# Performance work log

Hardware: AMD Instinct MI355X
Metric: run time of the kernel (lower is better)

## Reference

```python
import jax, jax.numpy as jnp
import numpy as np

SEQ_LEN = 12
BATCH = 2048
IN_DIM = 512
HIDDEN = 1024


def setup_inputs() -> dict:
    key = jax.random.key(0)
    k1, k2, k3, k4 = jax.random.split(key, 4)
    scale = 1.0 / np.sqrt(IN_DIM + HIDDEN)
    return {
        "x": jax.random.normal(k1, (BATCH, SEQ_LEN, IN_DIM), dtype=jnp.float32),
        "coded_cords": jax.random.normal(k2, (BATCH, HIDDEN), dtype=jnp.float32),
        # TF GRUCell fused gate kernel: [in+hidden, 2*hidden] (reset, update), bias init 1.0
        "gate_kernel": jax.random.normal(k3, (IN_DIM + HIDDEN, 2 * HIDDEN), dtype=jnp.float32) * scale,
        "gate_bias": jnp.ones((2 * HIDDEN,), dtype=jnp.float32),
        # candidate kernel: [in+hidden, hidden], zero bias
        "cand_kernel": jax.random.normal(k4, (IN_DIM + HIDDEN, HIDDEN), dtype=jnp.float32) * scale,
        "cand_bias": jnp.zeros((HIDDEN,), dtype=jnp.float32),
    }


def reference(x, coded_cords, gate_kernel, gate_bias, cand_kernel, cand_bias):
    # GRU recurrence (tf.contrib.rnn.GRUCell math), initial state = coded_cords.
    def step(h, xt):
        # xt: [B, D], h: [B, H]
        gates = jax.nn.sigmoid(jnp.concatenate([xt, h], axis=-1) @ gate_kernel + gate_bias)
        r, u = jnp.split(gates, 2, axis=-1)  # reset, update gates [B, H]
        c = jnp.tanh(jnp.concatenate([xt, r * h], axis=-1) @ cand_kernel + cand_bias)
        h_new = u * h + (1.0 - u) * c
        return h_new, h_new

    xs = jnp.swapaxes(x, 0, 1)  # [T, B, D]
    _, ys = jax.lax.scan(step, coded_cords, xs)  # ys: [T, B, H]
    return jnp.swapaxes(ys, 0, 1)  # [B, T, H]
```

## Files before the change

### kernel.cpp

```cpp
#include <hip/hip_runtime.h>
#include <hip/hip_bf16.h>


#define T_SEQ 12
#define BATCH 2048
#define IND 512
#define HID 1024
#define NGATE (2 * HID)
#define NPRE (NGATE + HID)

typedef __bf16 bf16x8 __attribute__((ext_vector_type(8)));
typedef __bf16 bf16x4 __attribute__((ext_vector_type(4)));
typedef float floatx4 __attribute__((ext_vector_type(4)));

#define AS1 __attribute__((address_space(1)))
#define AS3 __attribute__((address_space(3)))

__device__ __forceinline__ void gload16(const __bf16* g, __bf16* l) {
  __builtin_amdgcn_global_load_lds((const AS1 void*)g, (AS3 void*)l, 16, 0, 0);
}

__device__ __forceinline__ float fast_sigmoid(float v) {
  v = fminf(30.f, fmaxf(-30.f, v));
  return 1.f / (1.f + __expf(-v));
}
__device__ __forceinline__ float fast_tanh(float v) {
  v = fminf(15.f, fmaxf(-15.f, v));
  float e = __expf(2.f * v);
  return (e - 1.f) / (e + 1.f);
}

__global__ __launch_bounds__(256) void prep(
    const float* __restrict__ Wg, const float* __restrict__ Wc,
    const float* __restrict__ x, const float* __restrict__ coded,
    __bf16* __restrict__ Bx, __bf16* __restrict__ Bhg, __bf16* __restrict__ Bhc,
    __bf16* __restrict__ xb, float* __restrict__ h32, __bf16* __restrict__ hb) {
  int b = blockIdx.x;
  if (b < 2304) {
    int gid = b * 256 + threadIdx.x;
    int g = gid >> 6, lane = gid & 63;
    const float* W; int ld, row0, ksteps, wid; __bf16* out;
    if (g < 2048)      { W = Wg; ld = NGATE; row0 = 0;   ksteps = 16; wid = g;        out = Bx; }
    else if (g < 3072) { W = Wc; ld = HID;   row0 = 0;   ksteps = 16; wid = g - 2048; out = Bx + (size_t)2048 * 512; }
    else if (g < 7168) { W = Wg; ld = NGATE; row0 = IND; ksteps = 32; wid = g - 3072; out = Bhg; }
    else               { W = Wc; ld = HID;   row0 = IND; ksteps = 32; wid = g - 7168; out = Bhc; }
    int n16 = wid / ksteps, kt = wid - n16 * ksteps;
    int col = n16 * 16 + (lane & 15);
    int k0 = row0 + kt * 32 + (lane >> 4) * 8;
    bf16x8 v;
#pragma unroll
    for (int j = 0; j < 8; ++j) v[j] = (__bf16)W[(size_t)(k0 + j) * ld + col];
    *reinterpret_cast<bf16x8*>(out + (size_t)wid * 512 + lane * 8) = v;
  } else if (b < 4352) {
    int i = (b - 2304) * 256 + threadIdx.x;
    const float4* x4 = (const float4*)x;
    const int n4 = BATCH * T_SEQ * IND / 4;
    for (int k = i; k < n4; k += 2048 * 256) {
      float4 v = x4[k];
      bf16x4 o;
      o[0] = (__bf16)v.x; o[1] = (__bf16)v.y; o[2] = (__bf16)v.z; o[3] = (__bf16)v.w;
      *reinterpret_cast<bf16x4*>(xb + (size_t)k * 4) = o;
    }
  } else {
    int i = (b - 4352) * 256 + threadIdx.x;
    float4 v = ((const float4*)coded)[i];
    ((float4*)h32)[i] = v;
    bf16x4 o;
    o[0] = (__bf16)v.x; o[1] = (__bf16)v.y; o[2] = (__bf16)v.z; o[3] = (__bf16)v.w;
    *reinterpret_cast<bf16x4*>(hb + (size_t)i * 4) = o;
  }
}

__global__ __launch_bounds__(256) void pre_gemm(
    const __bf16* __restrict__ xb, const __bf16* __restrict__ Bx,
    const float* __restrict__ bg, const float* __restrict__ bc,
    __bf16* __restrict__ Pg, __bf16* __restrict__ Pc) {
  __shared__ __bf16 Alds[128 * 64];
  __shared__ __bf16 Blds[8192];
  const int tid = threadIdx.x, lane = tid & 63, w = tid >> 6;
  const int wm = w >> 1, wn = w & 1, quad = lane >> 4, l16 = lane & 15;
  const int bid = blockIdx.x;
  const int wg = (bid & 7) * 576 + (bid >> 3);
  const int nb = wg % 24;
  const int rest = wg / 24;
  const int mB = rest & 15;
  const int tz = rest >> 4;
  const int m0 = mB * 128;

  const __bf16* gA[4]; __bf16* lA[4];
  const __bf16* gB[4]; __bf16* lB[4];
#pragma unroll
  for (int i = 0; i < 4; ++i) {
    int c = tid + i * 256;
    int row = c >> 3, k8 = c & 7;
    gA[i] = xb + ((size_t)(m0 + row) * T_SEQ + tz) * IND + ((k8 ^ (row & 7)) * 8);
    lA[i] = Alds + c * 8;
    int ks2c = c >> 9, rem = c & 511;
    gB[i] = Bx + (((size_t)(nb * 8 + (rem >> 6)) * 16 + ks2c) * 64 + (rem & 63)) * 8;
    lB[i] = Blds + c * 8;
  }

  floatx4 acc[4][4] = {};
  for (int it = 0; it < 8; ++it) {
    __syncthreads();
#pragma unroll
    for (int i = 0; i < 4; ++i) gload16(gA[i] + it * 64, lA[i]);
#pragma unroll
    for (int i = 0; i < 4; ++i) gload16(gB[i] + (size_t)it * 1024, lB[i]);
    __syncthreads();
#pragma unroll
    for (int ks2 = 0; ks2 < 2; ++ks2) {
      bf16x8 af[4], bfr[4];
#pragma unroll
      for (int mf = 0; mf < 4; ++mf) {
        int row = wm * 64 + mf * 16 + l16;
        af[mf] = *(const bf16x8*)&Alds[row * 64 + (((ks2 * 4 + quad) ^ (row & 7)) * 8)];
      }
#pragma unroll
      for (int nf = 0; nf < 4; ++nf)
        bfr[nf] = *(const bf16x8*)&Blds[(ks2 * 512 + (wn * 4 + nf) * 64 + lane) * 8];
#pragma unroll
      for (int mf = 0; mf < 4; ++mf)
#pragma unroll
        for (int nf = 0; nf < 4; ++nf)
          acc[mf][nf] = __builtin_amdgcn_mfma_f32_16x16x32_bf16(af[mf], bfr[nf], acc[mf][nf], 0, 0, 0);
    }
  }

  const int n64g = nb * 2 + wn;
  const bool isg = (n64g < 32);
  __bf16* P = isg ? Pg : Pc;
  const float* bias = isg ? bg : bc;
  const int nrel = isg ? n64g : (n64g - 32);
  const int colb = nrel * 64 + l16;
#pragma unroll
  for (int mf = 0; mf < 4; ++mf) {
    int m32 = mB * 4 + wm * 2 + (mf >> 1);
    size_t tb = isg ? (((size_t)tz * 64 + m32) * 32 + n64g) * 2048
                    : (((size_t)tz * 64 + m32) * 16 + nrel) * 2048;
#pragma unroll
    for (int nf = 0; nf < 4; ++nf) {
      float bv = bias[colb + nf * 16];
      bf16x4 st;
#pragma unroll
      for (int i = 0; i < 4; ++i) st[i] = (__bf16)(acc[mf][nf][i] + bv);
      *(bf16x4*)&P[tb + (size_t)(((mf & 1) * 4 + nf) * 64 + lane) * 4] = st;
    }
  }
}

__global__ __launch_bounds__(256, 2) void gate_step(
    const __bf16* __restrict__ hb, const __bf16* __restrict__ Bhg,
    const __bf16* __restrict__ Pg, _Float16* __restrict__ u16,
    __bf16* __restrict__ rhb, int t) {
  __shared__ __bf16 Alds[64 * 64];
  __shared__ __bf16 Blds[8192];
  const int tid = threadIdx.x, lane = tid & 63, w = tid >> 6;
  const int wm = w >> 1, wn = w & 1, quad = lane >> 4, l16 = lane & 15;
  const int bid = blockIdx.x;
  const int swz = (bid & 7) * 64 + (bid >> 3);
  const int nT = swz & 15, mT = swz >> 4;

  const __bf16* gA[2];
  int ldsA[2];
#pragma unroll
  for (int i = 0; i < 2; ++i) {
    int c = tid + i * 256;
    gA[i] = hb + (size_t)(mT * 64 + (c >> 3)) * HID + (c & 7) * 8;
    ldsA[i] = (c >> 3) * 64 + (((c & 7) ^ ((c >> 3) & 7)) * 8);
  }
  const __bf16* gB[4];
  int ldsB[4];
#pragma unroll
  for (int i = 0; i < 4; ++i) {
    int c = tid + i * 256;
    int ks2c = c >> 9, rem = c & 511;
    gB[i] = Bhg + (((size_t)(nT * 8 + (rem >> 6)) * 32 + ks2c) * 64 + (rem & 63)) * 8;
    ldsB[i] = c * 8;
  }

  bf16x8 ra[4][2], rb[4][4];
#pragma unroll
  for (int s = 0; s < 4; ++s) {
#pragma unroll
    for (int i = 0; i < 2; ++i) ra[s][i] = *(const bf16x8*)(gA[i] + s * 64);
#pragma unroll
    for (int i = 0; i < 4; ++i) rb[s][i] = *(const bf16x8*)(gB[i] + (size_t)s * 1024);
  }

  floatx4 acc[2][4] = {};
#pragma unroll
  for (int it = 0; it < 16; ++it) {
    const int st = it & 3;
    __syncthreads();
#pragma unroll
    for (int i = 0; i < 2; ++i) *(bf16x8*)&Alds[ldsA[i]] = ra[st][i];
#pragma unroll
    for (int i = 0; i < 4; ++i) *(bf16x8*)&Blds[ldsB[i]] = rb[st][i];
    __syncthreads();
    if (it + 4 < 16) {
#pragma unroll
      for (int i = 0; i < 2; ++i) ra[st][i] = *(const bf16x8*)(gA[i] + (it + 4) * 64);
#pragma unroll
      for (int i = 0; i < 4; ++i) rb[st][i] = *(const bf16x8*)(gB[i] + (size_t)(it + 4) * 1024);
    }
#pragma unroll
    for (int ks2 = 0; ks2 < 2; ++ks2) {
      bf16x8 af[2], bfr[4];
#pragma unroll
      for (int mf = 0; mf < 2; ++mf) {
        int row = wm * 32 + mf * 16 + l16;
        af[mf] = *(const bf16x8*)&Alds[row * 64 + (((ks2 * 4 + quad) ^ (row & 7)) * 8)];
      }
#pragma unroll
      for (int nf = 0; nf < 4; ++nf)
        bfr[nf] = *(const bf16x8*)&Blds[(ks2 * 512 + (wn * 4 + nf) * 64 + lane) * 8];
#pragma unroll
      for (int mf = 0; mf < 2; ++mf)
#pragma unroll
        for (int nf = 0; nf < 4; ++nf)
          acc[mf][nf] = __builtin_amdgcn_mfma_f32_16x16x32_bf16(af[mf], bfr[nf], acc[mf][nf], 0, 0, 0);
    }
  }

  const int m32 = mT * 2 + wm;
  const int n64 = nT * 2 + wn;
  const bool isr = (n64 < 16);
  size_t tb = (((size_t)t * 64 + m32) * 32 + n64) * 2048;
#pragma unroll
  for (int mf = 0; mf < 2; ++mf)
#pragma unroll
    for (int nf = 0; nf < 4; ++nf) {
      bf16x4 px = *(const bf16x4*)&Pg[tb + (size_t)((mf * 4 + nf) * 64 + lane) * 4];
      int col = nT * 128 + wn * 64 + nf * 16 + l16;
      int rowb = mT * 64 + wm * 32 + mf * 16 + quad * 4;
#pragma unroll
      for (int i = 0; i < 4; ++i) {
        float s = fast_sigmoid(acc[mf][nf][i] + (float)px[i]);
        if (isr) {
          size_t idx = (size_t)(rowb + i) * HID + col;
          rhb[idx] = (__bf16)(s * (float)hb[idx]);
        } else {
          u16[(size_t)(rowb + i) * HID + (col - HID)] = (_Float16)s;
        }
      }
    }
}

__global__ __launch_bounds__(128, 2) void cand_step(
    const __bf16* __restrict__ rhb, const __bf16* __restrict__ Bhc,
    const __bf16* __restrict__ Pc, const _Float16* __restrict__ u16,
    float* __restrict__ h32, __bf16* __restrict__ hb,
    float* __restrict__ out, int t) {
  __shared__ __bf16 Alds[64 * 64];
  __shared__ __bf16 Blds[4096];
  const int tid = threadIdx.x, lane = tid & 63, wm = tid >> 6;
  const int quad = lane >> 4, l16 = lane & 15;
  const int bid = blockIdx.x;
  const int swz = (bid & 7) * 64 + (bid >> 3);
  const int nT = swz & 15, mT = swz >> 4;

  const __bf16* gA[4];
  int ldsA[4];
#pragma unroll
  for (int i = 0; i < 4; ++i) {
    int c = tid + i * 128;
    gA[i] = rhb + (size_t)(mT * 64 + (c >> 3)) * HID + (c & 7) * 8;
    ldsA[i] = (c >> 3) * 64 + (((c & 7) ^ ((c >> 3) & 7)) * 8);
  }
  const __bf16* gB[4];
  int ldsB[4];
#pragma unroll
  for (int i = 0; i < 4; ++i) {
    int c = tid + i * 128;
    int ks2c = c >> 8, rem = c & 255;
    gB[i] = Bhc + (((size_t)(nT * 4 + (rem >> 6)) * 32 + ks2c) * 64 + (rem & 63)) * 8;
    ldsB[i] = c * 8;
  }

  bf16x8 ra[4][4], rb[4][4];
#pragma unroll
  for (int s = 0; s < 4; ++s) {
#pragma unroll
    for (int i = 0; i < 4; ++i) {
      ra[s][i] = *(const bf16x8*)(gA[i] + s * 64);
      rb[s][i] = *(const bf16x8*)(gB[i] + (size_t)s * 1024);
    }
  }

  floatx4 acc[2][4] = {};
#pragma unroll
  for (int it = 0; it < 16; ++it) {
    const int st = it & 3;
    __syncthreads();
#pragma unroll
    for (int i = 0; i < 4; ++i) {
      *(bf16x8*)&Alds[ldsA[i]] = ra[st][i];
      *(bf16x8*)&Blds[ldsB[i]] = rb[st][i];
    }
    __syncthreads();
    if (it + 4 < 16) {
#pragma unroll
      for (int i = 0; i < 4; ++i) {
        ra[st][i] = *(const bf16x8*)(gA[i] + (it + 4) * 64);
        rb[st][i] = *(const bf16x8*)(gB[i] + (size_t)(it + 4) * 1024);
      }
    }
#pragma unroll
    for (int ks2 = 0; ks2 < 2; ++ks2) {
      bf16x8 af[2], bfr[4];
#pragma unroll
      for (int mf = 0; mf < 2; ++mf) {
        int row = wm * 32 + mf * 16 + l16;
        af[mf] = *(const bf16x8*)&Alds[row * 64 + (((ks2 * 4 + quad) ^ (row & 7)) * 8)];
      }
#pragma unroll
      for (int nf = 0; nf < 4; ++nf)
        bfr[nf] = *(const bf16x8*)&Blds[(ks2 * 256 + nf * 64 + lane) * 8];
#pragma unroll
      for (int mf = 0; mf < 2; ++mf)
#pragma unroll
        for (int nf = 0; nf < 4; ++nf)
          acc[mf][nf] = __builtin_amdgcn_mfma_f32_16x16x32_bf16(af[mf], bfr[nf], acc[mf][nf], 0, 0, 0);
    }
  }

  const int m32 = mT * 2 + wm;
  size_t tb = (((size_t)t * 64 + m32) * 16 + nT) * 2048;
#pragma unroll
  for (int mf = 0; mf < 2; ++mf)
#pragma unroll
    for (int nf = 0; nf < 4; ++nf) {
      bf16x4 px = *(const bf16x4*)&Pc[tb + (size_t)((mf * 4 + nf) * 64 + lane) * 4];
      int col = nT * 64 + nf * 16 + l16;
      int rowb = mT * 64 + wm * 32 + mf * 16 + quad * 4;
#pragma unroll
      for (int i = 0; i < 4; ++i) {
        float c = fast_tanh(acc[mf][nf][i] + (float)px[i]);
        size_t idx = (size_t)(rowb + i) * HID + col;
        float u = (float)u16[idx];
        float hnew = u * h32[idx] + (1.f - u) * c;
        h32[idx] = hnew;
        hb[idx] = (__bf16)hnew;
        __builtin_nontemporal_store(hnew, &out[(size_t)(rowb + i) * (T_SEQ * HID) + t * HID + col]);
      }
    }
}

extern "C" void kernel_launch(void* const* d_in, const int* in_sizes, int n_in,
                              void* d_out, int out_size, void* d_ws, size_t ws_size,
                              hipStream_t stream) {
  const float* x     = (const float*)d_in[0];
  const float* coded = (const float*)d_in[1];
  const float* Wg_f  = (const float*)d_in[2];
  const float* bg    = (const float*)d_in[3];
  const float* Wc_f  = (const float*)d_in[4];
  const float* bc    = (const float*)d_in[5];
  float* out = (float*)d_out;

  uintptr_t base = ((uintptr_t)d_ws + 255) & ~(uintptr_t)255;
  auto take = [&](size_t bytes) {
    void* p = (void*)base;
    base = (base + bytes + 255) & ~(uintptr_t)255;
    return p;
  };
  __bf16* Bx  = (__bf16*)take((size_t)(NPRE / 16) * 16 * 512 * 2);
  __bf16* Bhg = (__bf16*)take((size_t)(NGATE / 16) * 32 * 512 * 2);
  __bf16* Bhc = (__bf16*)take((size_t)(HID / 16) * 32 * 512 * 2);
  __bf16* Pg  = (__bf16*)take((size_t)T_SEQ * 64 * 32 * 2048 * 2);
  __bf16* Pc  = (__bf16*)take((size_t)T_SEQ * 64 * 16 * 2048 * 2);
  __bf16* xb  = (__bf16*)take((size_t)BATCH * T_SEQ * IND * 2);
  float*  h32 = (float*) take((size_t)BATCH * HID * 4);
  __bf16* hb  = (__bf16*)take((size_t)BATCH * HID * 2);
  _Float16* u16 = (_Float16*)take((size_t)BATCH * HID * 2);
  __bf16* rhb = (__bf16*)take((size_t)BATCH * HID * 2);

  prep<<<6400, 256, 0, stream>>>(Wg_f, Wc_f, x, coded, Bx, Bhg, Bhc, xb, h32, hb);

  pre_gemm<<<4608, 256, 0, stream>>>(xb, Bx, bg, bc, Pg, Pc);

  for (int t = 0; t < T_SEQ; ++t) {
    gate_step<<<512, 256, 0, stream>>>(hb, Bhg, Pg, u16, rhb, t);
    cand_step<<<512, 128, 0, stream>>>(rhb, Bhc, Pc, u16, h32, hb, out, t);
  }
}
```

Before: 807.2 us.

## Use direct global-to-LDS loads with larger K tiles in recurrent step GEMMs

Both per-step GEMM kernels drop the register-staged 4-deep prefetch pipeline. They now load 128-wide K tiles directly into LDS with global_load_lds, using a swizzled global address in place of a swizzled LDS address. The candidate kernel goes from 128 to 256 threads, with 4 waves splitting N so each computes a 32x32 output, and the block-to-tile swizzle now maps M fastest. This cuts register pressure and VGPR round-trips, but removes software prefetch overlap: each K tile is loaded and then waited on before compute. It also doubles LDS use per block.

```diff
diff --git a/kernel.cpp b/kernel.cpp
--- a/kernel.cpp
+++ b/kernel.cpp
@@ -153,68 +153,49 @@
     const __bf16* __restrict__ hb, const __bf16* __restrict__ Bhg,
     const __bf16* __restrict__ Pg, _Float16* __restrict__ u16,
     __bf16* __restrict__ rhb, int t) {
-  __shared__ __bf16 Alds[64 * 64];
-  __shared__ __bf16 Blds[8192];
+  __shared__ __bf16 Alds[64 * 128];
+  __shared__ __bf16 Blds[16384];
   const int tid = threadIdx.x, lane = tid & 63, w = tid >> 6;
   const int wm = w >> 1, wn = w & 1, quad = lane >> 4, l16 = lane & 15;
   const int bid = blockIdx.x;
   const int swz = (bid & 7) * 64 + (bid >> 3);
-  const int nT = swz & 15, mT = swz >> 4;
-
-  const __bf16* gA[2];
-  int ldsA[2];
-#pragma unroll
-  for (int i = 0; i < 2; ++i) {
-    int c = tid + i * 256;
-    gA[i] = hb + (size_t)(mT * 64 + (c >> 3)) * HID + (c & 7) * 8;
-    ldsA[i] = (c >> 3) * 64 + (((c & 7) ^ ((c >> 3) & 7)) * 8);
-  }
-  const __bf16* gB[4];
-  int ldsB[4];
+  const int mT = swz & 31, nT = swz >> 5;
+
+  const __bf16* gA[4]; __bf16* lA[4];
+  const __bf16* gB[8]; __bf16* lB[8];
 #pragma unroll
   for (int i = 0; i < 4; ++i) {
     int c = tid + i * 256;
-    int ks2c = c >> 9, rem = c & 511;
-    gB[i] = Bhg + (((size_t)(nT * 8 + (rem >> 6)) * 32 + ks2c) * 64 + (rem & 63)) * 8;
-    ldsB[i] = c * 8;
-  }
-
-  bf16x8 ra[4][2], rb[4][4];
-#pragma unroll
-  for (int s = 0; s < 4; ++s) {
-#pragma unroll
-    for (int i = 0; i < 2; ++i) ra[s][i] = *(const bf16x8*)(gA[i] + s * 64);
-#pragma unroll
-    for (int i = 0; i < 4; ++i) rb[s][i] = *(const bf16x8*)(gB[i] + (size_t)s * 1024);
+    int row = c >> 4, ch = c & 15;
+    gA[i] = hb + (size_t)(mT * 64 + row) * HID + ((ch ^ (row & 7)) * 8);
+    lA[i] = Alds + c * 8;
+  }
+#pragma unroll
+  for (int i = 0; i < 8; ++i) {
+    int c = tid + i * 256;
+    gB[i] = Bhg + (size_t)(nT * 8 + (c >> 8)) * 16384 + (c & 255) * 8;
+    lB[i] = Blds + c * 8;
   }
 
   floatx4 acc[2][4] = {};
-#pragma unroll
-  for (int it = 0; it < 16; ++it) {
-    const int st = it & 3;
-    __syncthreads();
-#pragma unroll
-    for (int i = 0; i < 2; ++i) *(bf16x8*)&Alds[ldsA[i]] = ra[st][i];
-#pragma unroll
-    for (int i = 0; i < 4; ++i) *(bf16x8*)&Blds[ldsB[i]] = rb[st][i];
-    __syncthreads();
-    if (it + 4 < 16) {
-#pragma unroll
-      for (int i = 0; i < 2; ++i) ra[st][i] = *(const bf16x8*)(gA[i] + (it + 4) * 64);
-#pragma unroll
-      for (int i = 0; i < 4; ++i) rb[st][i] = *(const bf16x8*)(gB[i] + (size_t)(it + 4) * 1024);
-    }
-#pragma unroll
-    for (int ks2 = 0; ks2 < 2; ++ks2) {
+  for (int kt = 0; kt < 8; ++kt) {
+    __syncthreads();
+#pragma unroll
+    for (int i = 0; i < 4; ++i) gload16(gA[i] + kt * 128, lA[i]);
+#pragma unroll
+    for (int i = 0; i < 8; ++i) gload16(gB[i] + kt * 2048, lB[i]);
+    __syncthreads();
+#pragma unroll
+    for (int ks2 = 0; ks2 < 4; ++ks2) {
       bf16x8 af[2], bfr[4];
 #pragma unroll
       for (int mf = 0; mf < 2; ++mf) {
         int row = wm * 32 + mf * 16 + l16;
-        af[mf] = *(const bf16x8*)&Alds[row * 64 + (((ks2 * 4 + quad) ^ (row & 7)) * 8)];
+        af[mf] = *(const bf16x8*)&Alds[row * 128 + (((ks2 * 4 + quad) ^ (row & 7)) * 8)];
       }
 #pragma unroll
       for (int nf = 0; nf < 4; ++nf)
-        bfr[nf] = *(const bf16x8*)&Blds[(ks2 * 512 + (wn * 4 + nf) * 64 + lane) * 8];
+        bfr[nf] = *(const bf16x8*)&Blds[(wn * 4 + nf) * 2048 + ks2 * 512 + lane * 8];
 #pragma unroll
       for (int mf = 0; mf < 2; ++mf)
 #pragma unroll
@@ -247,80 +228,54 @@
     }
 }
 
-__global__ __launch_bounds__(128, 2) void cand_step(
+__global__ __launch_bounds__(256, 2) void cand_step(
     const __bf16* __restrict__ rhb, const __bf16* __restrict__ Bhc,
     const __bf16* __restrict__ Pc, const _Float16* __restrict__ u16,
     float* __restrict__ h32, __bf16* __restrict__ hb,
     float* __restrict__ out, int t) {
-  __shared__ __bf16 Alds[64 * 64];
-  __shared__ __bf16 Blds[4096];
-  const int tid = threadIdx.x, lane = tid & 63, wm = tid >> 6;
-  const int quad = lane >> 4, l16 = lane & 15;
+  __shared__ __bf16 Alds[64 * 128];
+  __shared__ __bf16 Blds[8192];
+  const int tid = threadIdx.x, lane = tid & 63, w = tid >> 6;
+  const int wm = w >> 1, wn = w & 1, quad = lane >> 4, l16 = lane & 15;
   const int bid = blockIdx.x;
   const int swz = (bid & 7) * 64 + (bid >> 3);
-  const int nT = swz & 15, mT = swz >> 4;
-
-  const __bf16* gA[4];
-  int ldsA[4];
+  const int mT = swz & 31, nT = swz >> 5;
+
+  const __bf16* gA[4]; __bf16* lA[4];
+  const __bf16* gB[4]; __bf16* lB[4];
 #pragma unroll
   for (int i = 0; i < 4; ++i) {
-    int c = tid + i * 128;
-    gA[i] = rhb + (size_t)(mT * 64 + (c >> 3)) * HID + (c & 7) * 8;
-    ldsA[i] = (c >> 3) * 64 + (((c & 7) ^ ((c >> 3) & 7)) * 8);
-  }
-  const __bf16* gB[4];
-  int ldsB[4];
-#pragma unroll
-  for (int i = 0; i < 4; ++i) {
-    int c = tid + i * 128;
-    int ks2c = c >> 8, rem = c & 255;
-    gB[i] = Bhc + (((size_t)(nT * 4 + (rem >> 6)) * 32 + ks2c) * 64 + (rem & 63)) * 8;
-    ldsB[i] = c * 8;
-  }
-
-  bf16x8 ra[4][4], rb[4][4];
-#pragma unroll
-  for (int s = 0; s < 4; ++s) {
-#pragma unroll
-    for (int i = 0; i < 4; ++i) {
-      ra[s][i] = *(const bf16x8*)(gA[i] + s * 64);
-      rb[s][i] = *(const bf16x8*)(gB[i] + (size_t)s * 1024);
-    }
-  }
-
-  floatx4 acc[2][4] = {};
-#pragma unroll
-  for (int it = 0; it < 16; ++it) {
-    const int st = it & 3;
-    __syncthreads();
-#pragma unroll
-    for (int i = 0; i < 4; ++i) {
-      *(bf16x8*)&Alds[ldsA[i]] = ra[st][i];
-      *(bf16x8*)&Blds[ldsB[i]] = rb[st][i];
-    }
-    __syncthreads();
-    if (it + 4 < 16) {
-#pragma unroll
-      for (int i = 0; i < 4; ++i) {
-        ra[st][i] = *(const bf16x8*)(gA[i] + (it + 4) * 64);
-        rb[st][i] = *(const bf16x8*)(gB[i] + (size_t)(it + 4) * 1024);
-      }
-    }
-#pragma unroll
-    for (int ks2 = 0; ks2 < 2; ++ks2) {
-      bf16x8 af[2], bfr[4];
+    int c = tid + i * 256;
+    int row = c >> 4, ch = c & 15;
+    gA[i] = rhb + (size_t)(mT * 64 + row) * HID + ((ch ^ (row & 7)) * 8);
+    lA[i] = Alds + c * 8;
+    gB[i] = Bhc + (size_t)(nT * 4 + (c >> 8)) * 16384 + (c & 255) * 8;
+    lB[i] = Blds + c * 8;
+  }
+
+  floatx4 acc[2][2] = {};
+  for (int kt = 0; kt < 8; ++kt) {
+    __syncthreads();
+#pragma unroll
+    for (int i = 0; i < 4; ++i) gload16(gA[i] + kt * 128, lA[i]);
+#pragma unroll
+    for (int i = 0; i < 4; ++i) gload16(gB[i] + kt * 2048, lB[i]);
+    __syncthreads();
+#pragma unroll
+    for (int ks2 = 0; ks2 < 4; ++ks2) {
+      bf16x8 af[2], bfr[2];
 #pragma unroll
       for (int mf = 0; mf < 2; ++mf) {
         int row = wm * 32 + mf * 16 + l16;
-        af[mf] = *(const bf16x8*)&Alds[row * 64 + (((ks2 * 4 + quad) ^ (row & 7)) * 8)];
-      }
-#pragma unroll
-      for (int nf = 0; nf < 4; ++nf)
-        bfr[nf] = *(const bf16x8*)&Blds[(ks2 * 256 + nf * 64 + lane) * 8];
+        af[mf] = *(const bf16x8*)&Alds[row * 128 + (((ks2 * 4 + quad) ^ (row & 7)) * 8)];
+      }
+#pragma unroll
+      for (int nf = 0; nf < 2; ++nf)
+        bfr[nf] = *(const bf16x8*)&Blds[(wn * 2 + nf) * 2048 + ks2 * 512 + lane * 8];
 #pragma unroll
       for (int mf = 0; mf < 2; ++mf)
 #pragma unroll
-        for (int nf = 0; nf < 4; ++nf)
+        for (int nf = 0; nf < 2; ++nf)
           acc[mf][nf] = __builtin_amdgcn_mfma_f32_16x16x32_bf16(af[mf], bfr[nf], acc[mf][nf], 0, 0, 0);
     }
   }
@@ -330,9 +285,9 @@
 #pragma unroll
   for (int mf = 0; mf < 2; ++mf)
 #pragma unroll
-    for (int nf = 0; nf < 4; ++nf) {
-      bf16x4 px = *(const bf16x4*)&Pc[tb + (size_t)((mf * 4 + nf) * 64 + lane) * 4];
-      int col = nT * 64 + nf * 16 + l16;
+    for (int nf = 0; nf < 2; ++nf) {
+      bf16x4 px = *(const bf16x4*)&Pc[tb + (size_t)((mf * 4 + wn * 2 + nf) * 64 + lane) * 4];
+      int col = nT * 64 + wn * 32 + nf * 16 + l16;
       int rowb = mT * 64 + wm * 32 + mf * 16 + quad * 4;
 #pragma unroll
       for (int i = 0; i < 4; ++i) {
@@ -381,6 +336,6 @@
 
   for (int t = 0; t < T_SEQ; ++t) {
     gate_step<<<512, 256, 0, stream>>>(hb, Bhg, Pg, u16, rhb, t);
-    cand_step<<<512, 128, 0, stream>>>(rhb, Bhc, Pc, u16, h32, hb, out, t);
-  }
-}
+    cand_step<<<512, 256, 0, stream>>>(rhb, Bhc, Pc, u16, h32, hb, out, t);
+  }
+}
```

Result: faster. 734.9 us (-9.0%).
